# Kernel tuning notes

Measured on AMD Instinct MI355X. Metric: run time of the kernel, lower is better.

## Reference

```python
import jax, jax.numpy as jnp
import numpy as np

DIM = 1024
NUM_HEADS = 16
HEAD_DIM = DIM // NUM_HEADS
SCALE = HEAD_DIM ** -0.5


def setup_inputs() -> dict:
    key = jax.random.key(0)
    k1, k2, k3 = jax.random.split(key, 3)
    x = jax.random.normal(k1, (4, 2048, DIM), dtype=jnp.float32)
    w_qkv = jax.random.normal(k2, (DIM, 3 * DIM), dtype=jnp.float32) * (DIM ** -0.5)
    b_qkv = jnp.zeros((3 * DIM,), dtype=jnp.float32)
    w_proj = jax.random.normal(k3, (DIM, DIM), dtype=jnp.float32) * (DIM ** -0.5)
    b_proj = jnp.zeros((DIM,), dtype=jnp.float32)
    return {"x": x, "w_qkv": w_qkv, "b_qkv": b_qkv, "w_proj": w_proj, "b_proj": b_proj}


def reference(x, w_qkv, b_qkv, w_proj, b_proj):
    b, n, c = x.shape
    qkv = x @ w_qkv + b_qkv                       # [b, n, 3*dim]
    qkv = qkv.reshape(b, n, 3, NUM_HEADS, HEAD_DIM)
    qkv = jnp.transpose(qkv, (2, 0, 3, 1, 4))     # [3, b, H, n, hd]
    q, k, v = qkv[0], qkv[1], qkv[2]
    attn = jnp.einsum("bhqd,bhkd->bhqk", q, k) * SCALE
    attn = jax.nn.softmax(attn, axis=-1)
    out = jnp.einsum("bhqk,bhkd->bhqd", attn, v)  # [b, H, n, hd]
    out = jnp.transpose(out, (0, 2, 1, 3)).reshape(b, n, c)
    return out @ w_proj + b_proj
```

## Files before the change

kernel.cpp:

```cpp
#include <hip/hip_runtime.h>
#include <hip/hip_bf16.h>

typedef unsigned short u16;
typedef __attribute__((ext_vector_type(8))) short bf16x8;
typedef __attribute__((ext_vector_type(4))) float f32x4;
typedef __attribute__((ext_vector_type(16))) float f32x16;


__device__ __forceinline__ u16 f2bf(float f) {
  union { float f; unsigned u; } v; v.f = f;
  unsigned r = v.u + 0x7fffu + ((v.u >> 16) & 1u);
  return (u16)(r >> 16);
}

#if defined(__has_builtin)
#if __has_builtin(__builtin_amdgcn_cvt_pk_bf16_f32)
#define HAS_PK_BF16 1
#endif
#endif
__device__ __forceinline__ unsigned pk2bf(float a, float b) {
#ifdef HAS_PK_BF16
  typedef __attribute__((ext_vector_type(2))) __bf16 vbf2;
  union { vbf2 v; unsigned u; } u;
  u.v = __builtin_amdgcn_cvt_pk_bf16_f32(a, b);
  return u.u;
#else
  return (unsigned)f2bf(a) | ((unsigned)f2bf(b) << 16);
#endif
}

__device__ __forceinline__ f32x4 mfma16(bf16x8 a, bf16x8 b, f32x4 c) {
  return __builtin_amdgcn_mfma_f32_16x16x32_bf16(a, b, c, 0, 0, 0);
}
__device__ __forceinline__ f32x16 mfma32(bf16x8 a, bf16x8 b, f32x16 c) {
  return __builtin_amdgcn_mfma_f32_32x32x16_bf16(a, b, c, 0, 0, 0);
}

__device__ __forceinline__ void gl_lds16(const void* g, void* l) {
  __builtin_amdgcn_global_load_lds((__attribute__((address_space(1))) void*)g,
                                   (__attribute__((address_space(3))) void*)l,
                                   16, 0, 0);
}


__global__ void cvt_f32_bf16(const float* __restrict__ in, u16* __restrict__ out, int n) {
  int i = (blockIdx.x * blockDim.x + threadIdx.x) * 4;
  if (i >= n) return;
  float4 v = *(const float4*)(in + i);
  u16 o0 = f2bf(v.x), o1 = f2bf(v.y), o2 = f2bf(v.z), o3 = f2bf(v.w);
  ushort4 o; o.x = o0; o.y = o1; o.z = o2; o.w = o3;
  *(ushort4*)(out + i) = o;
}

__global__ void transpose_cvt(const float* __restrict__ in, u16* __restrict__ out,
                              int R, int C) {
  __shared__ u16 tile[64][65];
  int c0 = blockIdx.x * 64, r0 = blockIdx.y * 64;
  int lc = threadIdx.x & 63, lr = threadIdx.x >> 6;
#pragma unroll
  for (int i = 0; i < 16; ++i) {
    int r = lr + i * 4;
    tile[r][lc] = f2bf(in[(size_t)(r0 + r) * C + c0 + lc]);
  }
  __syncthreads();
#pragma unroll
  for (int i = 0; i < 16; ++i) {
    int c = lr + i * 4;
    out[(size_t)(c0 + c) * R + r0 + lc] = tile[lc][c];
  }
}


struct Smem256 { u16 A0[16384]; u16 B0[16384]; u16 A1[16384]; u16 B1[16384]; };

#define LDB128(base, off) (*(const bf16x8*)((const char*)(base) + (off)))
#define ISSUE(dst, p, j, k0) \
  gl_lds16((p) + (size_t)(j) * 65536 + (k0), (dst) + (j) * 4096 + dsel)

#define KSTEP(CA, CB, NA, NB, k0n, PF)                                           \
  do {                                                                           \
    bf16x8 aL[4][2], aH[4][2], bL[2][2], bH[2][2];                               \
        \
    _Pragma("unroll") for (int mi = 0; mi < 4; ++mi) {                           \
      aL[mi][0] = LDB128(CA, fA + mi * 2048 + cp0);                              \
      aL[mi][1] = LDB128(CA, fA + mi * 2048 + cp1);                              \
    }                                                                            \
    _Pragma("unroll") for (int ni = 0; ni < 2; ++ni) {                           \
      bL[ni][0] = LDB128(CB, fB + ni * 2048 + cp0);                              \
      bL[ni][1] = LDB128(CB, fB + ni * 2048 + cp1);                              \
    }                                                                            \
    if (PF) { ISSUE(NB, pB, 0, k0n); ISSUE(NB, pB, 1, k0n); }                    \
    __builtin_amdgcn_s_setprio(1);                                               \
    _Pragma("unroll") for (int mi = 0; mi < 4; ++mi)                             \
      _Pragma("unroll") for (int ni = 0; ni < 2; ++ni) {                         \
        acc[mi][ni] = mfma16(aL[mi][0], bL[ni][0], acc[mi][ni]);                 \
        acc[mi][ni] = mfma16(aL[mi][1], bL[ni][1], acc[mi][ni]);                 \
      }                                                                          \
    __builtin_amdgcn_s_setprio(0);                                               \
               \
    _Pragma("unroll") for (int ni = 0; ni < 2; ++ni) {                           \
      bH[ni][0] = LDB128(CB, fB + (ni + 2) * 2048 + cp0);                        \
      bH[ni][1] = LDB128(CB, fB + (ni + 2) * 2048 + cp1);                        \
    }                                                                            \
    if (PF) { ISSUE(NB, pB, 2, k0n); ISSUE(NB, pB, 3, k0n); }                    \
    __builtin_amdgcn_s_setprio(1);                                               \
    _Pragma("unroll") for (int mi = 0; mi < 4; ++mi)                             \
      _Pragma("unroll") for (int ni = 0; ni < 2; ++ni) {                         \
        acc[mi][ni + 2] = mfma16(aL[mi][0], bH[ni][0], acc[mi][ni + 2]);         \
        acc[mi][ni + 2] = mfma16(aL[mi][1], bH[ni][1], acc[mi][ni + 2]);         \
      }                                                                          \
    __builtin_amdgcn_s_setprio(0);                                               \
            \
    if (PF) asm volatile("s_waitcnt vmcnt(4)" ::: "memory");                     \
    else    asm volatile("s_waitcnt vmcnt(0)" ::: "memory");                     \
    __builtin_amdgcn_s_barrier();                                                \
    _Pragma("unroll") for (int mi = 0; mi < 4; ++mi) {                           \
      aH[mi][0] = LDB128(CA, fA + (mi + 4) * 2048 + cp0);                        \
      aH[mi][1] = LDB128(CA, fA + (mi + 4) * 2048 + cp1);                        \
    }                                                                            \
    if (PF) { ISSUE(NA, pA, 0, k0n); ISSUE(NA, pA, 2, k0n); }                    \
    __builtin_amdgcn_s_setprio(1);                                               \
    _Pragma("unroll") for (int mi = 0; mi < 4; ++mi)                             \
      _Pragma("unroll") for (int ni = 0; ni < 2; ++ni) {                         \
        acc[mi + 4][ni + 2] = mfma16(aH[mi][0], bH[ni][0], acc[mi + 4][ni + 2]); \
        acc[mi + 4][ni + 2] = mfma16(aH[mi][1], bH[ni][1], acc[mi + 4][ni + 2]); \
      }                                                                          \
    __builtin_amdgcn_s_setprio(0);                                               \
              \
    if (PF) { ISSUE(NA, pA, 1, k0n); ISSUE(NA, pA, 3, k0n); }                    \
    __builtin_amdgcn_s_setprio(1);                                               \
    _Pragma("unroll") for (int mi = 0; mi < 4; ++mi)                             \
      _Pragma("unroll") for (int ni = 0; ni < 2; ++ni) {                         \
        acc[mi + 4][ni] = mfma16(aH[mi][0], bL[ni][0], acc[mi + 4][ni]);         \
        acc[mi + 4][ni] = mfma16(aH[mi][1], bL[ni][1], acc[mi + 4][ni]);         \
      }                                                                          \
    __builtin_amdgcn_s_setprio(0);                                               \
    if (PF) asm volatile("s_waitcnt vmcnt(2)" ::: "memory");                     \
    __builtin_amdgcn_s_barrier();                                                \
  } while (0)

#define GEMM256_SETUP(Amat, Bmat)                                                \
  __shared__ Smem256 sm;                                                         \
  const int t = threadIdx.x, lane = t & 63, wave = t >> 6;                       \
  const int quad = lane >> 4, l15 = lane & 15;                                   \
  const int wm = wave >> 2, wn = wave & 3;                                       \
  const int row0 = blockIdx.x * 256, col0 = blockIdx.y * 256;                    \
  const int rowb = t >> 3, lc = (t & 7) ^ ((t >> 3) & 7);                        \
  const u16* pA = (Amat) + (size_t)(row0 + rowb) * 1024 + lc * 8;                \
  const u16* pB = (Bmat) + (size_t)(col0 + rowb) * 1024 + lc * 8;                \
  const size_t dsel = (size_t)wave * 512;                                        \
  const int fA = (wm * 128 + l15) * 128;                                         \
  const int fB = (wn * 64 + l15) * 128;                                          \
  const int cp0 = ((quad) ^ (l15 & 7)) << 4;                                     \
  const int cp1 = ((quad + 4) ^ (l15 & 7)) << 4;                                 \
  f32x4 acc[8][4] = {};                                                          \
  ISSUE(sm.B0, pB, 0, 0); ISSUE(sm.B0, pB, 1, 0);                                \
  ISSUE(sm.B0, pB, 2, 0); ISSUE(sm.B0, pB, 3, 0);                                \
  ISSUE(sm.A0, pA, 0, 0); ISSUE(sm.A0, pA, 2, 0);                                \
  ISSUE(sm.A0, pA, 1, 0); ISSUE(sm.A0, pA, 3, 0);                                \
  asm volatile("s_waitcnt vmcnt(2)" ::: "memory");                               \
  __builtin_amdgcn_s_barrier();                                                  \
  _Pragma("unroll 1")                                                            \
  for (int kk = 0; kk < 8; ++kk) {                                               \
    const int k0 = kk * 128;                                                     \
    KSTEP(sm.A0, sm.B0, sm.A1, sm.B1, k0 + 64, 1);                               \
    KSTEP(sm.A1, sm.B1, sm.A0, sm.B0, k0 + 128, (kk < 7));                       \
  }


__global__ __launch_bounds__(512, 2) void gemm_qkv(
    const u16* __restrict__ A, const u16* __restrict__ Bt,
    const float* __restrict__ bias,
    u16* __restrict__ Qb, u16* __restrict__ Kb, u16* __restrict__ Vt) {
  GEMM256_SETUP(A, Bt)

  const int which = col0 >> 10;

  if (which == 2) {
    u16* Ts = ((u16*)&sm) + wave * 8192;
#pragma unroll
    for (int ni = 0; ni < 4; ++ni) {
      const int d = ni * 16 + l15;
      const float bv = bias[col0 + wn * 64 + ni * 16 + l15];
#pragma unroll
      for (int mi = 0; mi < 8; ++mi) {
        const int s = mi * 16 + quad * 4;
        uint2 pk;
        pk.x = pk2bf(acc[mi][ni][0] + bv, acc[mi][ni][1] + bv);
        pk.y = pk2bf(acc[mi][ni][2] + bv, acc[mi][ni][3] + bv);
        *(uint2*)((char*)Ts + d * 256 + (((s >> 3) ^ (d & 15)) << 4) + (s & 4) * 2) = pk;
      }
    }
    const int h = ((col0 - 2048) >> 6) + wn;
    const int b_ = row0 >> 11;
    const int s0w = (row0 & 2047) + wm * 128;
    u16* vt = Vt + ((size_t)(b_ * 16 + h) * 64) * 2048;
#pragma unroll
    for (int it = 0; it < 16; ++it) {
      const int d = it * 4 + quad;
      uint4 v = *(const uint4*)((const char*)Ts + d * 256 + ((l15 ^ (d & 15)) << 4));
      *(uint4*)(vt + (size_t)d * 2048 + s0w + l15 * 8) = v;
    }
    return;
  }

  u16* dst = which == 0 ? Qb : Kb;
  const float qscale = which == 0 ? 0.1803368801111137f : 1.0f;
#pragma unroll
  for (int ni = 0; ni < 4; ++ni) {
    const int col = (col0 & 1023) + wn * 64 + ni * 16 + l15;
    const float bv = bias[col0 + wn * 64 + ni * 16 + l15];
    const int h = col >> 6, d = col & 63;
#pragma unroll
    for (int mi = 0; mi < 8; ++mi) {
#pragma unroll
      for (int r = 0; r < 4; ++r) {
        const int row = row0 + wm * 128 + mi * 16 + quad * 4 + r;
        const int bb = row >> 11, s = row & 2047;
        dst[(((size_t)bb * 16 + h) * 2048 + s) * 64 + d] =
            f2bf((acc[mi][ni][r] + bv) * qscale);
      }
    }
  }
}


__global__ __launch_bounds__(512, 2) void gemm_proj(
    const u16* __restrict__ A, const u16* __restrict__ Bt,
    const float* __restrict__ bias, float* __restrict__ C) {
  GEMM256_SETUP(A, Bt)

#pragma unroll
  for (int ni = 0; ni < 4; ++ni) {
    const int col = col0 + wn * 64 + ni * 16 + l15;
    const float bv = bias[col];
#pragma unroll
    for (int mi = 0; mi < 8; ++mi) {
#pragma unroll
      for (int r = 0; r < 4; ++r) {
        const int row = row0 + wm * 128 + mi * 16 + quad * 4 + r;
        C[(size_t)row * 1024 + col] = acc[mi][ni][r] + bv;
      }
    }
  }
}


__device__ __forceinline__ void softmax32(const f32x16& s, float& l,
                                          bf16x8& paA, bf16x8& paB) {
  unsigned D[8];
#pragma unroll
  for (int i = 0; i < 8; ++i) {
    float a = __builtin_amdgcn_exp2f(s[2 * i]);
    float b = __builtin_amdgcn_exp2f(s[2 * i + 1]);
    l += a + b;
    D[i] = pk2bf(a, b);
  }
  {
    unsigned x = D[0], x2 = D[1], y = D[2], y2 = D[3];
    asm volatile("v_permlane32_swap_b32 %0, %1" : "+v"(x), "+v"(y));
    asm volatile("v_permlane32_swap_b32 %0, %1" : "+v"(x2), "+v"(y2));
    union { unsigned u[4]; bf16x8 v; } p;
    p.u[0] = x; p.u[1] = x2; p.u[2] = y; p.u[3] = y2;
    paA = p.v;
  }
  {
    unsigned x = D[4], x2 = D[5], y = D[6], y2 = D[7];
    asm volatile("v_permlane32_swap_b32 %0, %1" : "+v"(x), "+v"(y));
    asm volatile("v_permlane32_swap_b32 %0, %1" : "+v"(x2), "+v"(y2));
    union { unsigned u[4]; bf16x8 v; } p;
    p.u[0] = x; p.u[1] = x2; p.u[2] = y; p.u[3] = y2;
    paB = p.v;
  }
}

__global__ __launch_bounds__(256, 2) void attn_kernel(
    const u16* __restrict__ Qb, const u16* __restrict__ Kb,
    const u16* __restrict__ Vt, u16* __restrict__ Ob) {
  __shared__ u16 KsA[64 * 64], KsB[64 * 64];
  __shared__ u16 VsA[64 * 64], VsB[64 * 64];
  const int bh = blockIdx.x, q0 = blockIdx.y * 256;
  const u16* Qp = Qb + (size_t)bh * 2048 * 64;
  const u16* Kp = Kb + (size_t)bh * 2048 * 64;
  const u16* Vp = Vt + (size_t)bh * 64 * 2048;
  const int t = threadIdx.x, lane = t & 63, wave = t >> 6;
  const int l31 = lane & 31, hi = lane >> 5;

  const int kr0 = t >> 3, kc0 = (t & 7) ^ (kr0 & 7);
  const int kr1 = (256 + t) >> 3, kc1 = ((256 + t) & 7) ^ (kr1 & 7);
  const u16* Kg0 = Kp + (size_t)kr0 * 64 + kc0 * 8;
  const u16* Kg1 = Kp + (size_t)kr1 * 64 + kc1 * 8;
  const u16* Vg0 = Vp + (size_t)kr0 * 2048 + kc0 * 8;
  const u16* Vg1 = Vp + (size_t)kr1 * 2048 + kc1 * 8;
  const size_t dof0 = (size_t)wave * 512;
  const size_t dof1 = 2048 + (size_t)wave * 512;

#define STAGE(Kd, Vd, key0)                                   \
  do {                                                        \
    gl_lds16(Kg0 + (size_t)(key0) * 64, (Kd) + dof0);         \
    gl_lds16(Kg1 + (size_t)(key0) * 64, (Kd) + dof1);         \
    gl_lds16(Vg0 + (key0), (Vd) + dof0);                      \
    gl_lds16(Vg1 + (key0), (Vd) + dof1);                      \
  } while (0)

  STAGE(KsA, VsA, 0);
  const u16* Qr0 = Qp + (size_t)(q0 + wave * 64 + l31) * 64 + hi * 8;
  const u16* Qr1 = Qr0 + 32 * 64;
  bf16x8 qf0[4], qf1[4];
#pragma unroll
  for (int dc = 0; dc < 4; ++dc) {
    qf0[dc] = *(const bf16x8*)(Qr0 + dc * 16);
    qf1[dc] = *(const bf16x8*)(Qr1 + dc * 16);
  }
  __syncthreads();

  const int rm = l31 & 7;
  int off[2][4];
#pragma unroll
  for (int x = 0; x < 2; ++x)
#pragma unroll
    for (int c = 0; c < 4; ++c)
      off[x][c] = x * 4096 + l31 * 128 + (((c * 2 + hi) ^ rm) << 4);

  f32x16 acc00 = {}, acc01 = {}, acc10 = {}, acc11 = {};
  float l0 = 0.f, l1 = 0.f;

#define TILE(Ks, Vs)                                                          \
  do {                                                                        \
    _Pragma("unroll")                                                         \
    for (int kh = 0; kh < 2; ++kh) {                                          \
      f32x16 s0 = {}, s1 = {};                                                \
      __builtin_amdgcn_s_setprio(1);                                          \
      _Pragma("unroll")                                                       \
      for (int dc = 0; dc < 4; ++dc) {                                        \
        bf16x8 kf = *(const bf16x8*)((const char*)(Ks) + off[kh][dc]);        \
        s0 = mfma32(kf, qf0[dc], s0);                                         \
        s1 = mfma32(kf, qf1[dc], s1);                                         \
      }                                                                       \
      __builtin_amdgcn_s_setprio(0);                                          \
      bf16x8 pa00, pa01, pa10, pa11;                                          \
      softmax32(s0, l0, pa00, pa01);                                          \
      softmax32(s1, l1, pa10, pa11);                                          \
      __builtin_amdgcn_s_setprio(1);                                          \
      _Pragma("unroll")                                                       \
      for (int ci = 0; ci < 2; ++ci) {                                        \
        const int c = 2 * kh + ci;                                            \
        bf16x8 vlo = *(const bf16x8*)((const char*)(Vs) + off[0][c]);         \
        bf16x8 vhiv = *(const bf16x8*)((const char*)(Vs) + off[1][c]);        \
        bf16x8 pa0 = ci ? pa01 : pa00;                                        \
        bf16x8 pa1 = ci ? pa11 : pa10;                                        \
        acc00 = mfma32(pa0, vlo, acc00);                                      \
        acc01 = mfma32(pa0, vhiv, acc01);                                     \
        acc10 = mfma32(pa1, vlo, acc10);                                      \
        acc11 = mfma32(pa1, vhiv, acc11);                                     \
      }                                                                       \
      __builtin_amdgcn_s_setprio(0);                                          \
    }                                                                         \
  } while (0)

#pragma unroll 1
  for (int kt2 = 0; kt2 < 16; ++kt2) {
    const int kt = kt2 * 2;
    STAGE(KsB, VsB, (kt + 1) * 64);
    TILE(KsA, VsA);
    __syncthreads();
    if (kt2 < 15) STAGE(KsA, VsA, (kt + 2) * 64);
    TILE(KsB, VsB);
    __syncthreads();
  }
#undef TILE
#undef STAGE

  l0 += __shfl_xor(l0, 32);
  l1 += __shfl_xor(l1, 32);
  float inv0 = 1.f / l0, inv1 = 1.f / l1;

  const int b_ = bh >> 4, h = bh & 15;
  const int qw = q0 + wave * 64;
#pragma unroll
  for (int r = 0; r < 16; ++r) {
    const int ql = (r & 3) + 8 * (r >> 2) + 4 * hi;
    float iv0 = __shfl(inv0, ql);
    float iv1 = __shfl(inv1, ql);
    size_t base0 = ((size_t)b_ * 2048 + qw + ql) * 1024 + h * 64;
    size_t base1 = base0 + (size_t)32 * 1024;
    Ob[base0 + l31] = f2bf(acc00[r] * iv0);
    Ob[base0 + 32 + l31] = f2bf(acc01[r] * iv0);
    Ob[base1 + l31] = f2bf(acc10[r] * iv1);
    Ob[base1 + 32 + l31] = f2bf(acc11[r] * iv1);
  }
}


extern "C" void kernel_launch(void* const* d_in, const int* in_sizes, int n_in,
                              void* d_out, int out_size, void* d_ws, size_t ws_size,
                              hipStream_t stream) {
  const float* x      = (const float*)d_in[0];
  const float* w_qkv  = (const float*)d_in[1];
  const float* b_qkv  = (const float*)d_in[2];
  const float* w_proj = (const float*)d_in[3];
  const float* b_proj = (const float*)d_in[4];
  float* out = (float*)d_out;
  char* ws = (char*)d_ws;

  u16* xb    = (u16*)(ws);
  u16* wqkvt = (u16*)(ws + 16777216);
  u16* wprjt = (u16*)(ws + 23068672);
  u16* Qb    = (u16*)(ws + 25165824);
  u16* Kb    = (u16*)(ws + 41943040);
  u16* Vt    = (u16*)(ws + 58720256);
  u16* Ob    = xb;
  if (ws_size < 92274688u) return;

  cvt_f32_bf16<<<8192, 256, 0, stream>>>(x, xb, 8388608);
  transpose_cvt<<<dim3(48, 16), 256, 0, stream>>>(w_qkv, wqkvt, 1024, 3072);
  transpose_cvt<<<dim3(16, 16), 256, 0, stream>>>(w_proj, wprjt, 1024, 1024);
  gemm_qkv<<<dim3(32, 12), 512, 0, stream>>>(xb, wqkvt, b_qkv, Qb, Kb, Vt);
  attn_kernel<<<dim3(64, 8), 256, 0, stream>>>(Qb, Kb, Vt, Ob);
  gemm_proj<<<dim3(32, 4), 512, 0, stream>>>(Ob, wprjt, b_proj, out);
}
```

Baseline: 270.6 us.

## Shrink GEMM tiles to 128x256 and merge weight transpose launches

The QKV and projection GEMMs now use 128-row tiles instead of 256-row tiles. This doubles the grid: the projection goes from 128 to 256 blocks and QKV from 384 to 768, which fills the CUs better on MI355X. The A-tile loads, LDS layout, prefetch wait counts and V-transpose epilogue are reworked to fit the smaller tile. The two weight transpose-convert launches are merged into one kernel to save a launch. Each block now reuses less data per tile, so global and LDS traffic per flop rises.

Measured after the change: 255.9 us. -5.4%, faster.

```diff
diff --git a/kernel.cpp b/kernel.cpp
--- a/kernel.cpp
+++ b/kernel.cpp
@@ -52,10 +52,15 @@
   *(ushort4*)(out + i) = o;
 }
 
-__global__ void transpose_cvt(const float* __restrict__ in, u16* __restrict__ out,
-                              int R, int C) {
+__global__ void transpose_cvt2(const float* __restrict__ wq, const float* __restrict__ wp,
+                               u16* __restrict__ oq, u16* __restrict__ op) {
   __shared__ u16 tile[64][65];
-  int c0 = blockIdx.x * 64, r0 = blockIdx.y * 64;
+  const int bx = blockIdx.x;
+  const float* in; u16* out; int C, c0;
+  if (bx < 48) { in = wq; out = oq; C = 3072; c0 = bx * 64; }
+  else         { in = wp; out = op; C = 1024; c0 = (bx - 48) * 64; }
+  const int R = 1024;
+  int r0 = blockIdx.y * 64;
   int lc = threadIdx.x & 63, lr = threadIdx.x >> 6;
 #pragma unroll
   for (int i = 0; i < 16; ++i) {
@@ -71,100 +76,101 @@
 }
 
 
-struct Smem256 { u16 A0[16384]; u16 B0[16384]; u16 A1[16384]; u16 B1[16384]; };
+struct Smem128 { u16 A0[8192]; u16 B0[16384]; u16 A1[8192]; u16 B1[16384]; };
 
 #define LDB128(base, off) (*(const bf16x8*)((const char*)(base) + (off)))
-#define ISSUE(dst, p, j, k0) \
-  gl_lds16((p) + (size_t)(j) * 65536 + (k0), (dst) + (j) * 4096 + dsel)
-
-#define KSTEP(CA, CB, NA, NB, k0n, PF)                                           \
-  do {                                                                           \
-    bf16x8 aL[4][2], aH[4][2], bL[2][2], bH[2][2];                               \
-        \
-    _Pragma("unroll") for (int mi = 0; mi < 4; ++mi) {                           \
-      aL[mi][0] = LDB128(CA, fA + mi * 2048 + cp0);                              \
-      aL[mi][1] = LDB128(CA, fA + mi * 2048 + cp1);                              \
-    }                                                                            \
-    _Pragma("unroll") for (int ni = 0; ni < 2; ++ni) {                           \
-      bL[ni][0] = LDB128(CB, fB + ni * 2048 + cp0);                              \
-      bL[ni][1] = LDB128(CB, fB + ni * 2048 + cp1);                              \
-    }                                                                            \
-    if (PF) { ISSUE(NB, pB, 0, k0n); ISSUE(NB, pB, 1, k0n); }                    \
-    __builtin_amdgcn_s_setprio(1);                                               \
-    _Pragma("unroll") for (int mi = 0; mi < 4; ++mi)                             \
-      _Pragma("unroll") for (int ni = 0; ni < 2; ++ni) {                         \
-        acc[mi][ni] = mfma16(aL[mi][0], bL[ni][0], acc[mi][ni]);                 \
-        acc[mi][ni] = mfma16(aL[mi][1], bL[ni][1], acc[mi][ni]);                 \
-      }                                                                          \
-    __builtin_amdgcn_s_setprio(0);                                               \
-               \
-    _Pragma("unroll") for (int ni = 0; ni < 2; ++ni) {                           \
-      bH[ni][0] = LDB128(CB, fB + (ni + 2) * 2048 + cp0);                        \
-      bH[ni][1] = LDB128(CB, fB + (ni + 2) * 2048 + cp1);                        \
-    }                                                                            \
-    if (PF) { ISSUE(NB, pB, 2, k0n); ISSUE(NB, pB, 3, k0n); }                    \
-    __builtin_amdgcn_s_setprio(1);                                               \
-    _Pragma("unroll") for (int mi = 0; mi < 4; ++mi)                             \
-      _Pragma("unroll") for (int ni = 0; ni < 2; ++ni) {                         \
-        acc[mi][ni + 2] = mfma16(aL[mi][0], bH[ni][0], acc[mi][ni + 2]);         \
-        acc[mi][ni + 2] = mfma16(aL[mi][1], bH[ni][1], acc[mi][ni + 2]);         \
-      }                                                                          \
-    __builtin_amdgcn_s_setprio(0);                                               \
+#define ISSUE_A(dst, j, k0) \
+  gl_lds16(pA + (size_t)(j) * 32768 + (k0), (dst) + (j) * 4096 + dsel)
+#define ISSUE_B(dst, j, k0) \
+  gl_lds16(pB + (size_t)(j) * 65536 + (k0), (dst) + (j) * 4096 + dsel)
+
+#define KSTEP(CA, CB, NA, NB, k0n, PF)                                         \
+  do {                                                                         \
+    bf16x8 aL[2][2], aH[2][2], bL[2][2], bH[2][2];                             \
             \
-    if (PF) asm volatile("s_waitcnt vmcnt(4)" ::: "memory");                     \
-    else    asm volatile("s_waitcnt vmcnt(0)" ::: "memory");                     \
-    __builtin_amdgcn_s_barrier();                                                \
-    _Pragma("unroll") for (int mi = 0; mi < 4; ++mi) {                           \
-      aH[mi][0] = LDB128(CA, fA + (mi + 4) * 2048 + cp0);                        \
-      aH[mi][1] = LDB128(CA, fA + (mi + 4) * 2048 + cp1);                        \
-    }                                                                            \
-    if (PF) { ISSUE(NA, pA, 0, k0n); ISSUE(NA, pA, 2, k0n); }                    \
-    __builtin_amdgcn_s_setprio(1);                                               \
-    _Pragma("unroll") for (int mi = 0; mi < 4; ++mi)                             \
-      _Pragma("unroll") for (int ni = 0; ni < 2; ++ni) {                         \
-        acc[mi + 4][ni + 2] = mfma16(aH[mi][0], bH[ni][0], acc[mi + 4][ni + 2]); \
-        acc[mi + 4][ni + 2] = mfma16(aH[mi][1], bH[ni][1], acc[mi + 4][ni + 2]); \
-      }                                                                          \
-    __builtin_amdgcn_s_setprio(0);                                               \
-              \
-    if (PF) { ISSUE(NA, pA, 1, k0n); ISSUE(NA, pA, 3, k0n); }                    \
-    __builtin_amdgcn_s_setprio(1);                                               \
-    _Pragma("unroll") for (int mi = 0; mi < 4; ++mi)                             \
-      _Pragma("unroll") for (int ni = 0; ni < 2; ++ni) {                         \
-        acc[mi + 4][ni] = mfma16(aH[mi][0], bL[ni][0], acc[mi + 4][ni]);         \
-        acc[mi + 4][ni] = mfma16(aH[mi][1], bL[ni][1], acc[mi + 4][ni]);         \
-      }                                                                          \
-    __builtin_amdgcn_s_setprio(0);                                               \
-    if (PF) asm volatile("s_waitcnt vmcnt(2)" ::: "memory");                     \
-    __builtin_amdgcn_s_barrier();                                                \
+    _Pragma("unroll") for (int mt = 0; mt < 2; ++mt) {                         \
+      aL[mt][0] = LDB128(CA, aoff + mt * 2048 + cp0);                          \
+      aL[mt][1] = LDB128(CA, aoff + mt * 2048 + cp1);                          \
+    }                                                                          \
+    _Pragma("unroll") for (int nt = 0; nt < 2; ++nt) {                         \
+      bL[nt][0] = LDB128(CB, boff + nt * 2048 + cp0);                          \
+      bL[nt][1] = LDB128(CB, boff + nt * 2048 + cp1);                          \
+    }                                                                          \
+    if (PF) { ISSUE_B(NB, 0, k0n); ISSUE_B(NB, 1, k0n); }                      \
+    __builtin_amdgcn_s_setprio(1);                                             \
+    _Pragma("unroll") for (int mt = 0; mt < 2; ++mt)                           \
+      _Pragma("unroll") for (int nt = 0; nt < 2; ++nt) {                       \
+        acc[mt][nt] = mfma16(aL[mt][0], bL[nt][0], acc[mt][nt]);               \
+        acc[mt][nt] = mfma16(aL[mt][1], bL[nt][1], acc[mt][nt]);               \
+      }                                                                        \
+    __builtin_amdgcn_s_setprio(0);                                             \
+                             \
+    _Pragma("unroll") for (int nt = 0; nt < 2; ++nt) {                         \
+      bH[nt][0] = LDB128(CB, boff + (nt + 2) * 2048 + cp0);                    \
+      bH[nt][1] = LDB128(CB, boff + (nt + 2) * 2048 + cp1);                    \
+    }                                                                          \
+    if (PF) { ISSUE_B(NB, 2, k0n); ISSUE_B(NB, 3, k0n); }                      \
+    __builtin_amdgcn_s_setprio(1);                                             \
+    _Pragma("unroll") for (int mt = 0; mt < 2; ++mt)                           \
+      _Pragma("unroll") for (int nt = 0; nt < 2; ++nt) {                       \
+        acc[mt][nt + 2] = mfma16(aL[mt][0], bH[nt][0], acc[mt][nt + 2]);       \
+        acc[mt][nt + 2] = mfma16(aL[mt][1], bH[nt][1], acc[mt][nt + 2]);       \
+      }                                                                        \
+    __builtin_amdgcn_s_setprio(0);                                             \
+       \
+    if (PF) asm volatile("s_waitcnt vmcnt(4)" ::: "memory");                   \
+    else    asm volatile("s_waitcnt vmcnt(0)" ::: "memory");                   \
+    __builtin_amdgcn_s_barrier();                                              \
+    _Pragma("unroll") for (int mt = 0; mt < 2; ++mt) {                         \
+      aH[mt][0] = LDB128(CA, 8192 + aoff + mt * 2048 + cp0);                   \
+      aH[mt][1] = LDB128(CA, 8192 + aoff + mt * 2048 + cp1);                   \
+    }                                                                          \
+    if (PF) ISSUE_A(NA, 0, k0n);                                               \
+    __builtin_amdgcn_s_setprio(1);                                             \
+    _Pragma("unroll") for (int mt = 0; mt < 2; ++mt)                           \
+      _Pragma("unroll") for (int nt = 0; nt < 2; ++nt) {                       \
+        acc[mt + 2][nt + 2] = mfma16(aH[mt][0], bH[nt][0], acc[mt + 2][nt + 2]); \
+        acc[mt + 2][nt + 2] = mfma16(aH[mt][1], bH[nt][1], acc[mt + 2][nt + 2]); \
+      }                                                                        \
+    __builtin_amdgcn_s_setprio(0);                                             \
+                   \
+    if (PF) ISSUE_A(NA, 1, k0n);                                               \
+    __builtin_amdgcn_s_setprio(1);                                             \
+    _Pragma("unroll") for (int mt = 0; mt < 2; ++mt)                           \
+      _Pragma("unroll") for (int nt = 0; nt < 2; ++nt) {                       \
+        acc[mt + 2][nt] = mfma16(aH[mt][0], bL[nt][0], acc[mt + 2][nt]);       \
+        acc[mt + 2][nt] = mfma16(aH[mt][1], bL[nt][1], acc[mt + 2][nt]);       \
+      }                                                                        \
+    __builtin_amdgcn_s_setprio(0);                                             \
+    if (PF) asm volatile("s_waitcnt vmcnt(1)" ::: "memory");                   \
+    __builtin_amdgcn_s_barrier();                                              \
   } while (0)
 
-#define GEMM256_SETUP(Amat, Bmat)                                                \
-  __shared__ Smem256 sm;                                                         \
-  const int t = threadIdx.x, lane = t & 63, wave = t >> 6;                       \
-  const int quad = lane >> 4, l15 = lane & 15;                                   \
-  const int wm = wave >> 2, wn = wave & 3;                                       \
-  const int row0 = blockIdx.x * 256, col0 = blockIdx.y * 256;                    \
-  const int rowb = t >> 3, lc = (t & 7) ^ ((t >> 3) & 7);                        \
-  const u16* pA = (Amat) + (size_t)(row0 + rowb) * 1024 + lc * 8;                \
-  const u16* pB = (Bmat) + (size_t)(col0 + rowb) * 1024 + lc * 8;                \
-  const size_t dsel = (size_t)wave * 512;                                        \
-  const int fA = (wm * 128 + l15) * 128;                                         \
-  const int fB = (wn * 64 + l15) * 128;                                          \
-  const int cp0 = ((quad) ^ (l15 & 7)) << 4;                                     \
-  const int cp1 = ((quad + 4) ^ (l15 & 7)) << 4;                                 \
-  f32x4 acc[8][4] = {};                                                          \
-  ISSUE(sm.B0, pB, 0, 0); ISSUE(sm.B0, pB, 1, 0);                                \
-  ISSUE(sm.B0, pB, 2, 0); ISSUE(sm.B0, pB, 3, 0);                                \
-  ISSUE(sm.A0, pA, 0, 0); ISSUE(sm.A0, pA, 2, 0);                                \
-  ISSUE(sm.A0, pA, 1, 0); ISSUE(sm.A0, pA, 3, 0);                                \
-  asm volatile("s_waitcnt vmcnt(2)" ::: "memory");                               \
-  __builtin_amdgcn_s_barrier();                                                  \
-  _Pragma("unroll 1")                                                            \
-  for (int kk = 0; kk < 8; ++kk) {                                               \
-    const int k0 = kk * 128;                                                     \
-    KSTEP(sm.A0, sm.B0, sm.A1, sm.B1, k0 + 64, 1);                               \
-    KSTEP(sm.A1, sm.B1, sm.A0, sm.B0, k0 + 128, (kk < 7));                       \
+#define GEMM128_SETUP(Amat, Bmat)                                              \
+  __shared__ Smem128 sm;                                                       \
+  const int t = threadIdx.x, lane = t & 63, wave = t >> 6;                     \
+  const int quad = lane >> 4, l15 = lane & 15;                                 \
+  const int wm = wave >> 2, wn = wave & 3;                                     \
+  const int row0 = blockIdx.x * 128, col0 = blockIdx.y * 256;                  \
+  const int g = t >> 3, f0 = g + (g & 32);      \
+  const int swz = (t & 7) ^ (g & 7);                                           \
+  const u16* pA = (Amat) + (size_t)(row0 + f0) * 1024 + swz * 8;               \
+  const u16* pB = (Bmat) + (size_t)(col0 + g) * 1024 + swz * 8;                \
+  const size_t dsel = (size_t)wave * 512;                                      \
+  const int rm = l15 & 7;                                                      \
+  const int aoff = wm * 4096 + l15 * 128;                                      \
+  const int boff = (wn * 64 + l15) * 128;                                      \
+  const int cp0 = (quad ^ rm) << 4, cp1 = ((quad + 4) ^ rm) << 4;              \
+  f32x4 acc[4][4] = {};                                                        \
+  ISSUE_B(sm.B0, 0, 0); ISSUE_B(sm.B0, 1, 0);                                  \
+  ISSUE_B(sm.B0, 2, 0); ISSUE_B(sm.B0, 3, 0);                                  \
+  ISSUE_A(sm.A0, 0, 0); ISSUE_A(sm.A0, 1, 0);                                  \
+  asm volatile("s_waitcnt vmcnt(1)" ::: "memory");                             \
+  __builtin_amdgcn_s_barrier();                                                \
+  _Pragma("unroll 1")                                                          \
+  for (int kk = 0; kk < 8; ++kk) {                                             \
+    KSTEP(sm.A0, sm.B0, sm.A1, sm.B1, (2 * kk + 1) * 64, 1);                   \
+    KSTEP(sm.A1, sm.B1, sm.A0, sm.B0, (2 * kk + 2) * 64, (kk < 7));            \
   }
 
 
@@ -172,34 +178,34 @@
     const u16* __restrict__ A, const u16* __restrict__ Bt,
     const float* __restrict__ bias,
     u16* __restrict__ Qb, u16* __restrict__ Kb, u16* __restrict__ Vt) {
-  GEMM256_SETUP(A, Bt)
+  GEMM128_SETUP(A, Bt)
 
   const int which = col0 >> 10;
 
   if (which == 2) {
-    u16* Ts = ((u16*)&sm) + wave * 8192;
-#pragma unroll
-    for (int ni = 0; ni < 4; ++ni) {
-      const int d = ni * 16 + l15;
-      const float bv = bias[col0 + wn * 64 + ni * 16 + l15];
-#pragma unroll
-      for (int mi = 0; mi < 8; ++mi) {
-        const int s = mi * 16 + quad * 4;
+    u16* Ts = ((u16*)&sm) + wave * 4096;
+#pragma unroll
+    for (int nt = 0; nt < 4; ++nt) {
+      const int d = nt * 16 + l15;
+      const float bv = bias[col0 + wn * 64 + nt * 16 + l15];
+#pragma unroll
+      for (int mt = 0; mt < 4; ++mt) {
         uint2 pk;
-        pk.x = pk2bf(acc[mi][ni][0] + bv, acc[mi][ni][1] + bv);
-        pk.y = pk2bf(acc[mi][ni][2] + bv, acc[mi][ni][3] + bv);
-        *(uint2*)((char*)Ts + d * 256 + (((s >> 3) ^ (d & 15)) << 4) + (s & 4) * 2) = pk;
+        pk.x = pk2bf(acc[mt][nt][0] + bv, acc[mt][nt][1] + bv);
+        pk.y = pk2bf(acc[mt][nt][2] + bv, acc[mt][nt][3] + bv);
+        *(uint2*)((char*)Ts + d * 128 +
+                  (((mt * 4 + quad) ^ ((d & 7) << 1)) << 3)) = pk;
       }
     }
     const int h = ((col0 - 2048) >> 6) + wn;
     const int b_ = row0 >> 11;
-    const int s0w = (row0 & 2047) + wm * 128;
-    u16* vt = Vt + ((size_t)(b_ * 16 + h) * 64) * 2048;
-#pragma unroll
-    for (int it = 0; it < 16; ++it) {
-      const int d = it * 4 + quad;
-      uint4 v = *(const uint4*)((const char*)Ts + d * 256 + ((l15 ^ (d & 15)) << 4));
-      *(uint4*)(vt + (size_t)d * 2048 + s0w + l15 * 8) = v;
+    const int s0w = (row0 & 2047) + wm * 64;
+    u16* vt = Vt + (size_t)(b_ * 16 + h) * 64 * 2048;
+#pragma unroll
+    for (int i = 0; i < 8; ++i) {
+      const int d = i * 8 + (lane >> 3), c = lane & 7;
+      uint4 v = *(const uint4*)((const char*)Ts + d * 128 + ((c ^ (d & 7)) << 4));
+      *(uint4*)(vt + (size_t)d * 2048 + s0w + c * 8) = v;
     }
     return;
   }
@@ -207,18 +213,18 @@
   u16* dst = which == 0 ? Qb : Kb;
   const float qscale = which == 0 ? 0.1803368801111137f : 1.0f;
 #pragma unroll
-  for (int ni = 0; ni < 4; ++ni) {
-    const int col = (col0 & 1023) + wn * 64 + ni * 16 + l15;
-    const float bv = bias[col0 + wn * 64 + ni * 16 + l15];
+  for (int nt = 0; nt < 4; ++nt) {
+    const int col = (col0 & 1023) + wn * 64 + nt * 16 + l15;
+    const float bv = bias[col0 + wn * 64 + nt * 16 + l15];
     const int h = col >> 6, d = col & 63;
 #pragma unroll
-    for (int mi = 0; mi < 8; ++mi) {
+    for (int mt = 0; mt < 4; ++mt) {
 #pragma unroll
       for (int r = 0; r < 4; ++r) {
-        const int row = row0 + wm * 128 + mi * 16 + quad * 4 + r;
+        const int row = row0 + wm * 64 + mt * 16 + quad * 4 + r;
         const int bb = row >> 11, s = row & 2047;
         dst[(((size_t)bb * 16 + h) * 2048 + s) * 64 + d] =
-            f2bf((acc[mi][ni][r] + bv) * qscale);
+            f2bf((acc[mt][nt][r] + bv) * qscale);
       }
     }
   }
@@ -228,18 +234,18 @@
 __global__ __launch_bounds__(512, 2) void gemm_proj(
     const u16* __restrict__ A, const u16* __restrict__ Bt,
     const float* __restrict__ bias, float* __restrict__ C) {
-  GEMM256_SETUP(A, Bt)
-
-#pragma unroll
-  for (int ni = 0; ni < 4; ++ni) {
-    const int col = col0 + wn * 64 + ni * 16 + l15;
+  GEMM128_SETUP(A, Bt)
+
+#pragma unroll
+  for (int nt = 0; nt < 4; ++nt) {
+    const int col = col0 + wn * 64 + nt * 16 + l15;
     const float bv = bias[col];
 #pragma unroll
-    for (int mi = 0; mi < 8; ++mi) {
+    for (int mt = 0; mt < 4; ++mt) {
 #pragma unroll
       for (int r = 0; r < 4; ++r) {
-        const int row = row0 + wm * 128 + mi * 16 + quad * 4 + r;
-        C[(size_t)row * 1024 + col] = acc[mi][ni][r] + bv;
+        const int row = row0 + wm * 64 + mt * 16 + quad * 4 + r;
+        C[(size_t)row * 1024 + col] = acc[mt][nt][r] + bv;
       }
     }
   }
@@ -413,9 +419,8 @@
   if (ws_size < 92274688u) return;
 
   cvt_f32_bf16<<<8192, 256, 0, stream>>>(x, xb, 8388608);
-  transpose_cvt<<<dim3(48, 16), 256, 0, stream>>>(w_qkv, wqkvt, 1024, 3072);
-  transpose_cvt<<<dim3(16, 16), 256, 0, stream>>>(w_proj, wprjt, 1024, 1024);
-  gemm_qkv<<<dim3(32, 12), 512, 0, stream>>>(xb, wqkvt, b_qkv, Qb, Kb, Vt);
+  transpose_cvt2<<<dim3(64, 16), 256, 0, stream>>>(w_qkv, w_proj, wqkvt, wprjt);
+  gemm_qkv<<<dim3(64, 12), 512, 0, stream>>>(xb, wqkvt, b_qkv, Qb, Kb, Vt);
   attn_kernel<<<dim3(64, 8), 256, 0, stream>>>(Qb, Kb, Vt, Ob);
-  gemm_proj<<<dim3(32, 4), 512, 0, stream>>>(Ob, wprjt, b_proj, out);
-}
+  gemm_proj<<<dim3(64, 4), 512, 0, stream>>>(Ob, wprjt, b_proj, out);
+}
```
